# Optimization experiments

Measured on AMD Instinct MI355X. Metric: run time of the kernel, lower is better.

## Reference

```python
import jax, jax.numpy as jnp
import numpy as np

NUM_EMBEDDINGS = 1024
EMBEDDING_DIM = 64
COMMITMENT_COST = 0.25


def setup_inputs() -> dict:
    key = jax.random.key(0)
    k1, k2 = jax.random.split(key)
    inputs = jax.random.normal(k1, (64, 32, 32, EMBEDDING_DIM), dtype=jnp.float32)
    # torch init is uniform(-1/K, 1/K); scale accordingly
    weight = jax.random.uniform(
        k2, (NUM_EMBEDDINGS, EMBEDDING_DIM), dtype=jnp.float32,
        minval=-1.0 / NUM_EMBEDDINGS, maxval=1.0 / NUM_EMBEDDINGS)
    return {"inputs": inputs, "weight": weight}


def reference(inputs, weight):
    input_shape = inputs.shape
    flat = inputs.reshape(-1, EMBEDDING_DIM)               # [N, D]
    distances = (jnp.sum(flat ** 2, axis=1, keepdims=True)
                 + jnp.sum(weight ** 2, axis=1)
                 - 2.0 * flat @ weight.T)                   # [N, K]
    encoding_indices = jnp.argmin(distances, axis=1)        # [N]
    # gather codes (equivalent to one-hot @ weight, but as a direct gather)
    quantized = weight[encoding_indices].reshape(input_shape)

    e_latent_loss = jnp.mean((jax.lax.stop_gradient(quantized) - inputs) ** 2)
    q_latent_loss = jnp.mean((quantized - jax.lax.stop_gradient(inputs)) ** 2)
    loss = q_latent_loss + COMMITMENT_COST * e_latent_loss

    # straight-through estimator
    quantized_ste = inputs + jax.lax.stop_gradient(quantized - inputs)

    # perplexity (equivalent to mean over the one-hot encodings)
    n_tokens = flat.shape[0]
    counts = jax.ops.segment_sum(
        jnp.ones((n_tokens,), jnp.float32), encoding_indices,
        num_segments=NUM_EMBEDDINGS)
    avg_probs = counts / n_tokens
    perplexity = jnp.exp(-jnp.sum(avg_probs * jnp.log(avg_probs + 1e-10)))

    indices_for_transformer = encoding_indices.reshape(input_shape[0], -1)
    return (loss, quantized_ste, perplexity, indices_for_transformer)
```

## Files before the change

kernel.cpp:

```cpp
#include <hip/hip_runtime.h>
#include <cstdint>
#include <cstddef>

#define N_TOKENS 65536
#define DIM 64
#define K_CODES 1024
#define NTH 256

#define OFF_Q 1
#define OFF_PERP 4194305
#define OFF_IDX 4194306

#define MARGIN 1.5e-4f

#define WS_LOSS   0
#define WS_FCNT   8
#define WS_COUNTS 16
#define WS_WHI    4112
#define WS_WLO    135184
#define WS_S2     266256
#define WS_FLIST  270352

typedef __attribute__((ext_vector_type(8))) short  s16x8;
typedef __attribute__((ext_vector_type(4))) float  f32x4;

__device__ __forceinline__ float fmulr(float a, float b){ return __fmul_rn(a,b); }
__device__ __forceinline__ float faddr(float a, float b){ return __fadd_rn(a,b); }

__device__ __forceinline__ unsigned short f2bf(float f) {
    unsigned u = __float_as_uint(f);
    unsigned r = u + 0x7fffu + ((u >> 16) & 1u);
    return (unsigned short)(r >> 16);
}
__device__ __forceinline__ float bf2f(unsigned short h) {
    return __uint_as_float(((unsigned)h) << 16);
}
__device__ __forceinline__ unsigned keyf(float f) {
    unsigned u = __float_as_uint(f);
    return u ^ ((u & 0x80000000u) ? 0xffffffffu : 0x80000000u);
}

__device__ float sumsq64_np(const float* __restrict__ p) {
    float s[16];
    #pragma unroll
    for (int l = 0; l < 16; ++l) {
        float a0 = fmulr(p[l],      p[l]);
        float a1 = fmulr(p[l + 16], p[l + 16]);
        float a2 = fmulr(p[l + 32], p[l + 32]);
        float a3 = fmulr(p[l + 48], p[l + 48]);
        s[l] = faddr(faddr(a0, a1), faddr(a2, a3));
    }
    #pragma unroll
    for (int len = 8; len >= 1; len >>= 1)
        #pragma unroll
        for (int l = 0; l < len; ++l)
            s[l] = faddr(s[l], s[l + len]);
    return s[0];
}

__device__ __forceinline__ void async_copy16(const void* g, void* l) {
    __builtin_amdgcn_global_load_lds(
        (const __attribute__((address_space(1))) void*)g,
        (__attribute__((address_space(3))) void*)l, 16, 0, 0);
}

__global__ void vq_prep(const float* __restrict__ W, unsigned short* __restrict__ Whi,
                        unsigned short* __restrict__ Wlo, float* __restrict__ s2g,
                        int* __restrict__ counts, int* __restrict__ gfcount,
                        double* __restrict__ loss_acc) {
    int gid = blockIdx.x * NTH + threadIdx.x;
    for (int e = gid; e < K_CODES * DIM; e += 16384) {
        float x = W[e];
        unsigned short hi = f2bf(x);
        unsigned short lo = f2bf(__fsub_rn(x, bf2f(hi)));
        int j = e >> 6, k = e & 63;
        int pos = j * 64 + (((k >> 3) ^ (j & 7)) << 3) + (k & 7);
        Whi[pos] = hi; Wlo[pos] = lo;
    }
    if (gid < K_CODES) { s2g[gid] = sumsq64_np(W + gid * 64); counts[gid] = 0; }
    if (gid == 0) { *loss_acc = 0.0; *gfcount = 0; }
}

__global__ __launch_bounds__(NTH, 3)
void vq_main(const float* __restrict__ X, const float* __restrict__ W,
             const unsigned short* __restrict__ WhiG, const unsigned short* __restrict__ WloG,
             const float* __restrict__ s2g, float* __restrict__ out,
             double* __restrict__ loss_acc, int* __restrict__ counts,
             int* __restrict__ gfcount, unsigned short* __restrict__ gflist) {
    __shared__ __align__(16) unsigned short xs_hi[64 * 64];
    __shared__ __align__(16) unsigned short xs_lo[64 * 64];
    __shared__ __align__(16) unsigned short ws_hi[128 * 64];
    __shared__ __align__(16) unsigned short ws_lo[128 * 64];
    __shared__ int fidx[64];
    __shared__ int flist[64];
    __shared__ int fcount, gbaseS;
    __shared__ double lred[4];

    const int tid  = threadIdx.x;
    const int lane = tid & 63, wave = tid >> 6;
    const int quad = lane >> 4, lrow = lane & 15;
    const int t0   = blockIdx.x * 64;

    if (tid == 0) fcount = 0;

    #pragma unroll
    for (int i = 0; i < 2; ++i) {
        int g = tid + NTH * i;
        int t = g >> 3, kb = g & 7;
        const float* src = X + (size_t)(t0 + t) * DIM + kb * 8;
        float v[8];
        *(f32x4*)v       = *(const f32x4*)src;
        *(f32x4*)(v + 4) = *(const f32x4*)(src + 4);
        unsigned short h[8], l[8];
        #pragma unroll
        for (int k = 0; k < 8; ++k) {
            h[k] = f2bf(v[k]);
            l[k] = f2bf(__fsub_rn(v[k], bf2f(h[k])));
        }
        int base = t * 64 + ((kb ^ (t & 7)) << 3);
        *(s16x8*)&xs_hi[base] = *(s16x8*)h;
        *(s16x8*)&xs_lo[base] = *(s16x8*)l;
    }
    __syncthreads();

    const int tf = wave * 16 + lrow;
    const int sA = tf & 7;
    s16x8 a_h0 = *(const s16x8*)&xs_hi[tf * 64 + (((0 + quad) ^ sA) << 3)];
    s16x8 a_h1 = *(const s16x8*)&xs_hi[tf * 64 + (((4 + quad) ^ sA) << 3)];
    s16x8 a_l0 = *(const s16x8*)&xs_lo[tf * 64 + (((0 + quad) ^ sA) << 3)];
    s16x8 a_l1 = *(const s16x8*)&xs_lo[tf * 64 + (((4 + quad) ^ sA) << 3)];

    float r1v[4], r2v[4]; int r1i[4];
    #pragma unroll
    for (int r = 0; r < 4; ++r) { r1v[r] = 3.4e38f; r2v[r] = 3.4e38f; r1i[r] = 0x7fffffff; }

    for (int ch = 0; ch < 8; ++ch) {
        __syncthreads();
        {
            const char* ghb = (const char*)WhiG + ch * 16384;
            const char* glb = (const char*)WloG + ch * 16384;
            char* lhb = (char*)ws_hi + wave * 1024;
            char* llb = (char*)ws_lo + wave * 1024;
            #pragma unroll
            for (int i = 0; i < 4; ++i) {
                int off = i * 4096 + tid * 16;
                async_copy16(ghb + off, lhb + i * 4096);
                async_copy16(glb + off, llb + i * 4096);
            }
        }
        __syncthreads();

        #pragma unroll
        for (int g = 0; g < 2; ++g) {
            #pragma unroll
            for (int t4 = 0; t4 < 4; ++t4) {
                int jl = g * 64 + t4 * 16 + lrow;
                int sB = jl & 7;
                s16x8 b_h0 = *(const s16x8*)&ws_hi[jl * 64 + (((0 + quad) ^ sB) << 3)];
                s16x8 b_h1 = *(const s16x8*)&ws_hi[jl * 64 + (((4 + quad) ^ sB) << 3)];
                s16x8 b_l0 = *(const s16x8*)&ws_lo[jl * 64 + (((0 + quad) ^ sB) << 3)];
                s16x8 b_l1 = *(const s16x8*)&ws_lo[jl * 64 + (((4 + quad) ^ sB) << 3)];
                f32x4 acc = {0.f, 0.f, 0.f, 0.f};
                acc = __builtin_amdgcn_mfma_f32_16x16x32_bf16(a_h0, b_h0, acc, 0, 0, 0);
                acc = __builtin_amdgcn_mfma_f32_16x16x32_bf16(a_h1, b_h1, acc, 0, 0, 0);
                acc = __builtin_amdgcn_mfma_f32_16x16x32_bf16(a_h0, b_l0, acc, 0, 0, 0);
                acc = __builtin_amdgcn_mfma_f32_16x16x32_bf16(a_h1, b_l1, acc, 0, 0, 0);
                acc = __builtin_amdgcn_mfma_f32_16x16x32_bf16(a_l0, b_h0, acc, 0, 0, 0);
                acc = __builtin_amdgcn_mfma_f32_16x16x32_bf16(a_l1, b_h1, acc, 0, 0, 0);
                int jcode = ch * 128 + jl;
                float s2v = s2g[jcode];
                #pragma unroll
                for (int r = 0; r < 4; ++r) {
                    float d = __builtin_fmaf(-2.0f, acc[r], s2v);
                    bool lt = d < r1v[r];
                    float old1 = r1v[r];
                    float sec  = lt ? old1 : d;
                    r2v[r] = fminf(r2v[r], sec);
                    r1v[r] = lt ? d : r1v[r];
                    r1i[r] = lt ? jcode : r1i[r];
                }
            }
        }
    }

    #pragma unroll
    for (int m = 1; m <= 8; m <<= 1) {
        #pragma unroll
        for (int r = 0; r < 4; ++r) {
            float o1v = __shfl_xor(r1v[r], m, 64);
            int   o1i = __shfl_xor(r1i[r], m, 64);
            float o2v = __shfl_xor(r2v[r], m, 64);
            bool take = (o1v < r1v[r]) || (o1v == r1v[r] && o1i < r1i[r]);
            float loser = take ? r1v[r] : o1v;
            r2v[r] = fminf(fminf(r2v[r], o2v), loser);
            if (take) { r1v[r] = o1v; r1i[r] = o1i; }
        }
    }
    if (lrow == 0) {
        #pragma unroll
        for (int r = 0; r < 4; ++r) {
            int t = wave * 16 + quad * 4 + r;
            bool fb = (r2v[r] - r1v[r]) < MARGIN;
            fidx[t] = fb ? (r1i[r] | (int)0x80000000) : r1i[r];
            if (fb) { int p = atomicAdd(&fcount, 1); flist[p] = t; }
        }
    }
    __syncthreads();

    double lsum = 0.0;
    #pragma unroll
    for (int i = 0; i < 16; ++i) {
        int e = tid + NTH * i;
        int t = e >> 6, dd = e & 63;
        int iv = fidx[t];
        if (iv >= 0) {
            float q = W[iv * 64 + dd];
            float x = X[(size_t)(t0 + t) * 64 + dd];
            out[(size_t)OFF_Q + (size_t)(t0 + t) * 64 + dd] = q;
            float df = __fsub_rn(q, x);
            lsum += (double)fmulr(df, df);
        }
    }
    #pragma unroll
    for (int off = 32; off >= 1; off >>= 1) lsum += __shfl_down(lsum, off, 64);
    if (lane == 0) lred[wave] = lsum;
    if (tid < 64) {
        int iv = fidx[tid];
        if (iv >= 0) {
            atomicAdd(&counts[iv], 1);
            out[(size_t)OFF_IDX + t0 + tid] = (float)iv;
        }
    }
    if (tid == 0) gbaseS = atomicAdd(gfcount, fcount);
    __syncthreads();
    if (tid < fcount) gflist[gbaseS + tid] = (unsigned short)(t0 + flist[tid]);
    if (tid == 0) atomicAdd(loss_acc, lred[0] + lred[1] + lred[2] + lred[3]);
}

#define FGT 16
#define FBC 256

__global__ __launch_bounds__(NTH, 2)
void vq_fallback(const float* __restrict__ X, const float* __restrict__ W,
                 const float* __restrict__ s2g, const int* __restrict__ gfcount,
                 const unsigned short* __restrict__ gflist, float* __restrict__ out,
                 double* __restrict__ loss_acc, int* __restrict__ counts) {
    int count = *gfcount;
    int base = blockIdx.x * FGT;
    if (base >= count) return;
    int nt = min(FGT, count - base);

    __shared__ __align__(16) float xsf[FGT * 64];
    __shared__ __align__(16) float wsf[FBC * 64];
    __shared__ float s1f[FGT];
    __shared__ unsigned long long redf[FGT * 32];
    __shared__ int gidx[FGT];
    __shared__ double lredf[4];

    const int tid = threadIdx.x;
    const int lane = tid & 63, wave = tid >> 6;
    const int r = tid & 7, c = tid >> 3;

    if (tid < nt * 16) {
        int t = tid >> 4, kb4 = tid & 15;
        int tok = gflist[base + t];
        f32x4 v = *(const f32x4*)(X + (size_t)tok * 64 + kb4 * 4);
        *(f32x4*)&xsf[t * 64 + ((kb4 ^ (t & 7)) << 2)] = v;
    }
    if (tid < nt) s1f[tid] = sumsq64_np(X + (size_t)gflist[base + tid] * 64);

    unsigned long long best0 = ~0ULL, best1 = ~0ULL;
    const int ta = 2 * r, tb = 2 * r + 1;

    for (int ch = 0; ch < K_CODES / FBC; ++ch) {
        __syncthreads();
        #pragma unroll
        for (int i = 0; i < 16; ++i) {
            int e = tid + NTH * i;
            int jl = e >> 4, kb4 = e & 15;
            f32x4 v = *(const f32x4*)(W + (size_t)(ch * FBC + jl) * 64 + kb4 * 4);
            *(f32x4*)&wsf[jl * 64 + ((kb4 ^ ((jl >> 3) & 7)) << 2)] = v;
        }
        __syncthreads();

        float acc[2][8];
        #pragma unroll
        for (int m = 0; m < 8; ++m) { acc[0][m] = 0.f; acc[1][m] = 0.f; }

        #pragma unroll
        for (int kb4 = 0; kb4 < 16; ++kb4) {
            f32x4 xa = *(const f32x4*)&xsf[ta * 64 + ((kb4 ^ (ta & 7)) << 2)];
            f32x4 xb = *(const f32x4*)&xsf[tb * 64 + ((kb4 ^ (tb & 7)) << 2)];
            #pragma unroll
            for (int m = 0; m < 8; ++m) {
                int jl = 8 * c + m;
                f32x4 wv = *(const f32x4*)&wsf[jl * 64 + ((kb4 ^ (c & 7)) << 2)];
                acc[0][m] = __builtin_fmaf(xa[0], wv[0], acc[0][m]);
                acc[0][m] = __builtin_fmaf(xa[1], wv[1], acc[0][m]);
                acc[0][m] = __builtin_fmaf(xa[2], wv[2], acc[0][m]);
                acc[0][m] = __builtin_fmaf(xa[3], wv[3], acc[0][m]);
                acc[1][m] = __builtin_fmaf(xb[0], wv[0], acc[1][m]);
                acc[1][m] = __builtin_fmaf(xb[1], wv[1], acc[1][m]);
                acc[1][m] = __builtin_fmaf(xb[2], wv[2], acc[1][m]);
                acc[1][m] = __builtin_fmaf(xb[3], wv[3], acc[1][m]);
            }
        }
        #pragma unroll
        for (int m = 0; m < 8; ++m) {
            int jcode = ch * FBC + 8 * c + m;
            float s2v = s2g[jcode];
            float d0 = faddr(faddr(s1f[ta], s2v), fmulr(-2.0f, acc[0][m]));
            float d1 = faddr(faddr(s1f[tb], s2v), fmulr(-2.0f, acc[1][m]));
            unsigned long long p0 = ((unsigned long long)keyf(d0) << 32) | (unsigned)jcode;
            unsigned long long p1 = ((unsigned long long)keyf(d1) << 32) | (unsigned)jcode;
            best0 = p0 < best0 ? p0 : best0;
            best1 = p1 < best1 ? p1 : best1;
        }
    }
    redf[ta * 32 + c] = best0;
    redf[tb * 32 + c] = best1;
    __syncthreads();
    if (tid < FGT) {
        unsigned long long b = redf[tid * 32];
        #pragma unroll
        for (int cc = 1; cc < 32; ++cc) {
            unsigned long long v = redf[tid * 32 + cc];
            b = v < b ? v : b;
        }
        int idx = (int)(b & 0xffffffffu);
        gidx[tid] = idx;
        if (tid < nt) {
            int tok = gflist[base + tid];
            out[(size_t)OFF_IDX + tok] = (float)idx;
            atomicAdd(&counts[idx], 1);
        }
    }
    __syncthreads();
    double lsum = 0.0;
    #pragma unroll
    for (int i = 0; i < 4; ++i) {
        int e = tid + NTH * i;
        int t = e >> 6, dd = e & 63;
        if (t < nt) {
            int tok = gflist[base + t];
            int idx = gidx[t];
            float q = W[idx * 64 + dd];
            float x = X[(size_t)tok * 64 + dd];
            out[(size_t)OFF_Q + (size_t)tok * 64 + dd] = q;
            float df = __fsub_rn(q, x);
            lsum += (double)fmulr(df, df);
        }
    }
    #pragma unroll
    for (int off = 32; off >= 1; off >>= 1) lsum += __shfl_down(lsum, off, 64);
    if (lane == 0) lredf[wave] = lsum;
    __syncthreads();
    if (tid == 0) atomicAdd(loss_acc, lredf[0] + lredf[1] + lredf[2] + lredf[3]);
}

__global__ void vq_final(const int* __restrict__ counts,
                         const double* __restrict__ loss_acc,
                         float* __restrict__ out) {
    __shared__ double hred[4];
    int tid = threadIdx.x;
    double h = 0.0;
    for (int j = tid; j < K_CODES; j += 256) {
        double p = (double)counts[j] / 65536.0;
        h += p * log(p + 1e-10);
    }
    #pragma unroll
    for (int off = 32; off >= 1; off >>= 1) h += __shfl_down(h, off, 64);
    if ((tid & 63) == 0) hred[tid >> 6] = h;
    __syncthreads();
    if (tid == 0) {
        double H = hred[0] + hred[1] + hred[2] + hred[3];
        out[OFF_PERP] = (float)exp(-H);
        double ls = *loss_acc;
        float Lf = (float)(ls / 4194304.0);
        out[0] = faddr(Lf, fmulr(0.25f, Lf));
    }
}

extern "C" void kernel_launch(void* const* d_in, const int* in_sizes, int n_in,
                              void* d_out, int out_size, void* d_ws, size_t ws_size,
                              hipStream_t stream) {
    const float* X = (const float*)d_in[0];
    const float* W = (const float*)d_in[1];
    float* out = (float*)d_out;
    char* ws = (char*)d_ws;
    double* loss_acc = (double*)(ws + WS_LOSS);
    int* gfcount = (int*)(ws + WS_FCNT);
    int* counts = (int*)(ws + WS_COUNTS);
    unsigned short* Whi = (unsigned short*)(ws + WS_WHI);
    unsigned short* Wlo = (unsigned short*)(ws + WS_WLO);
    float* s2g = (float*)(ws + WS_S2);
    unsigned short* gflist = (unsigned short*)(ws + WS_FLIST);

    vq_prep<<<64, NTH, 0, stream>>>(W, Whi, Wlo, s2g, counts, gfcount, loss_acc);
    vq_main<<<N_TOKENS / 64, NTH, 0, stream>>>(X, W, Whi, Wlo, s2g, out,
                                               loss_acc, counts, gfcount, gflist);
    vq_fallback<<<N_TOKENS / FGT, NTH, 0, stream>>>(X, W, s2g, gfcount, gflist,
                                                    out, loss_acc, counts);
    vq_final<<<1, NTH, 0, stream>>>(counts, loss_acc, out);
}
```

Before: 177.3 us.

## Double-buffer codebook chunks, 128 tokens per block, retile fallback kernel

The main kernel now handles 128 tokens per block, with two 16-row A fragments per wave, so each codebook tile loaded into LDS is reused twice. Codebook chunks are 64 codes and double-buffered with async copies, so the next chunk loads while the current one computes, and each chunk iteration needs one barrier instead of two. The -0.5*||e||^2 term is folded into the MFMA accumulator init, and the per-code norms are staged once in LDS. The fallback kernel is retiled to 64 tokens x 128 codes with 4x8 register blocking, and the epilogue loads and stores are vectorised to float4. The cost is more registers and LDS per block (occupancy hint lowered from 3 to 2) and half as many main-kernel blocks.

```diff
diff --git a/kernel.cpp b/kernel.cpp
--- a/kernel.cpp
+++ b/kernel.cpp
@@ -6,6 +6,8 @@
 #define DIM 64
 #define K_CODES 1024
 #define NTH 256
+#define TPB 128
+#define NCH 16
 
 #define OFF_Q 1
 #define OFF_PERP 4194305
@@ -34,10 +36,6 @@
 }
 __device__ __forceinline__ float bf2f(unsigned short h) {
     return __uint_as_float(((unsigned)h) << 16);
-}
-__device__ __forceinline__ unsigned keyf(float f) {
-    unsigned u = __float_as_uint(f);
-    return u ^ ((u & 0x80000000u) ? 0xffffffffu : 0x80000000u);
 }
 
 __device__ float sumsq64_np(const float* __restrict__ p) {
@@ -81,30 +79,43 @@
     if (gid == 0) { *loss_acc = 0.0; *gfcount = 0; }
 }
 
-__global__ __launch_bounds__(NTH, 3)
+__global__ __launch_bounds__(NTH, 2)
 void vq_main(const float* __restrict__ X, const float* __restrict__ W,
              const unsigned short* __restrict__ WhiG, const unsigned short* __restrict__ WloG,
              const float* __restrict__ s2g, float* __restrict__ out,
              double* __restrict__ loss_acc, int* __restrict__ counts,
              int* __restrict__ gfcount, unsigned short* __restrict__ gflist) {
-    __shared__ __align__(16) unsigned short xs_hi[64 * 64];
-    __shared__ __align__(16) unsigned short xs_lo[64 * 64];
-    __shared__ __align__(16) unsigned short ws_hi[128 * 64];
-    __shared__ __align__(16) unsigned short ws_lo[128 * 64];
-    __shared__ int fidx[64];
-    __shared__ int flist[64];
+    __shared__ __align__(16) unsigned short xs_hi[TPB * 64];
+    __shared__ __align__(16) unsigned short xs_lo[TPB * 64];
+    __shared__ __align__(16) unsigned short ws_hi[2][64 * 64];
+    __shared__ __align__(16) unsigned short ws_lo[2][64 * 64];
+    __shared__ __align__(16) float s2s[K_CODES];
+    __shared__ int fidx[TPB];
+    __shared__ int flist[TPB];
     __shared__ int fcount, gbaseS;
     __shared__ double lred[4];
 
     const int tid  = threadIdx.x;
     const int lane = tid & 63, wave = tid >> 6;
     const int quad = lane >> 4, lrow = lane & 15;
-    const int t0   = blockIdx.x * 64;
+    const int t0   = blockIdx.x * TPB;
 
     if (tid == 0) fcount = 0;
 
-    #pragma unroll
-    for (int i = 0; i < 2; ++i) {
+    {
+        const char* gh = (const char*)WhiG;
+        const char* gl = (const char*)WloG;
+        char* lh = (char*)&ws_hi[0][0] + wave * 1024;
+        char* ll = (char*)&ws_lo[0][0] + wave * 1024;
+        #pragma unroll
+        for (int i = 0; i < 2; ++i) {
+            async_copy16(gh + i * 4096 + tid * 16, lh + i * 4096);
+            async_copy16(gl + i * 4096 + tid * 16, ll + i * 4096);
+        }
+    }
+    *(f32x4*)&s2s[tid * 4] = *(const f32x4*)&s2g[tid * 4];
+    #pragma unroll
+    for (int i = 0; i < 4; ++i) {
         int g = tid + NTH * i;
         int t = g >> 3, kb = g & 7;
         const float* src = X + (size_t)(t0 + t) * DIM + kb * 8;
@@ -123,85 +134,91 @@
     }
     __syncthreads();
 
-    const int tf = wave * 16 + lrow;
-    const int sA = tf & 7;
-    s16x8 a_h0 = *(const s16x8*)&xs_hi[tf * 64 + (((0 + quad) ^ sA) << 3)];
-    s16x8 a_h1 = *(const s16x8*)&xs_hi[tf * 64 + (((4 + quad) ^ sA) << 3)];
-    s16x8 a_l0 = *(const s16x8*)&xs_lo[tf * 64 + (((0 + quad) ^ sA) << 3)];
-    s16x8 a_l1 = *(const s16x8*)&xs_lo[tf * 64 + (((4 + quad) ^ sA) << 3)];
-
-    float r1v[4], r2v[4]; int r1i[4];
-    #pragma unroll
-    for (int r = 0; r < 4; ++r) { r1v[r] = 3.4e38f; r2v[r] = 3.4e38f; r1i[r] = 0x7fffffff; }
-
-    for (int ch = 0; ch < 8; ++ch) {
-        __syncthreads();
-        {
-            const char* ghb = (const char*)WhiG + ch * 16384;
-            const char* glb = (const char*)WloG + ch * 16384;
-            char* lhb = (char*)ws_hi + wave * 1024;
-            char* llb = (char*)ws_lo + wave * 1024;
-            #pragma unroll
-            for (int i = 0; i < 4; ++i) {
-                int off = i * 4096 + tid * 16;
-                async_copy16(ghb + off, lhb + i * 4096);
-                async_copy16(glb + off, llb + i * 4096);
+    s16x8 a_h0[2], a_h1[2], a_l0[2], a_l1[2];
+    #pragma unroll
+    for (int rt = 0; rt < 2; ++rt) {
+        int tf = wave * 32 + rt * 16 + lrow;
+        int sA = tf & 7;
+        a_h0[rt] = *(const s16x8*)&xs_hi[tf * 64 + (((0 + quad) ^ sA) << 3)];
+        a_h1[rt] = *(const s16x8*)&xs_hi[tf * 64 + (((4 + quad) ^ sA) << 3)];
+        a_l0[rt] = *(const s16x8*)&xs_lo[tf * 64 + (((0 + quad) ^ sA) << 3)];
+        a_l1[rt] = *(const s16x8*)&xs_lo[tf * 64 + (((4 + quad) ^ sA) << 3)];
+    }
+
+    float r1v[8], r2v[8]; int r1i[8];
+    #pragma unroll
+    for (int ri = 0; ri < 8; ++ri) { r1v[ri] = 3.4e38f; r2v[ri] = 3.4e38f; r1i[ri] = 0x7fffffff; }
+
+    for (int ch = 0; ch < NCH; ++ch) {
+        const int buf = ch & 1;
+        if (ch < NCH - 1) {
+            const char* gh = (const char*)WhiG + (ch + 1) * 8192;
+            const char* gl = (const char*)WloG + (ch + 1) * 8192;
+            char* lh = (char*)&ws_hi[buf ^ 1][0] + wave * 1024;
+            char* ll = (char*)&ws_lo[buf ^ 1][0] + wave * 1024;
+            #pragma unroll
+            for (int i = 0; i < 2; ++i) {
+                async_copy16(gh + i * 4096 + tid * 16, lh + i * 4096);
+                async_copy16(gl + i * 4096 + tid * 16, ll + i * 4096);
             }
         }
-        __syncthreads();
-
-        #pragma unroll
-        for (int g = 0; g < 2; ++g) {
-            #pragma unroll
-            for (int t4 = 0; t4 < 4; ++t4) {
-                int jl = g * 64 + t4 * 16 + lrow;
-                int sB = jl & 7;
-                s16x8 b_h0 = *(const s16x8*)&ws_hi[jl * 64 + (((0 + quad) ^ sB) << 3)];
-                s16x8 b_h1 = *(const s16x8*)&ws_hi[jl * 64 + (((4 + quad) ^ sB) << 3)];
-                s16x8 b_l0 = *(const s16x8*)&ws_lo[jl * 64 + (((0 + quad) ^ sB) << 3)];
-                s16x8 b_l1 = *(const s16x8*)&ws_lo[jl * 64 + (((4 + quad) ^ sB) << 3)];
-                f32x4 acc = {0.f, 0.f, 0.f, 0.f};
-                acc = __builtin_amdgcn_mfma_f32_16x16x32_bf16(a_h0, b_h0, acc, 0, 0, 0);
-                acc = __builtin_amdgcn_mfma_f32_16x16x32_bf16(a_h1, b_h1, acc, 0, 0, 0);
-                acc = __builtin_amdgcn_mfma_f32_16x16x32_bf16(a_h0, b_l0, acc, 0, 0, 0);
-                acc = __builtin_amdgcn_mfma_f32_16x16x32_bf16(a_h1, b_l1, acc, 0, 0, 0);
-                acc = __builtin_amdgcn_mfma_f32_16x16x32_bf16(a_l0, b_h0, acc, 0, 0, 0);
-                acc = __builtin_amdgcn_mfma_f32_16x16x32_bf16(a_l1, b_h1, acc, 0, 0, 0);
-                int jcode = ch * 128 + jl;
-                float s2v = s2g[jcode];
+        #pragma unroll
+        for (int ct = 0; ct < 4; ++ct) {
+            int lc = ct * 16 + lrow;
+            int sB = lrow & 7;
+            const unsigned short* bh = &ws_hi[buf][lc * 64];
+            const unsigned short* bl = &ws_lo[buf][lc * 64];
+            s16x8 b_h0 = *(const s16x8*)&bh[((0 + quad) ^ sB) << 3];
+            s16x8 b_h1 = *(const s16x8*)&bh[((4 + quad) ^ sB) << 3];
+            s16x8 b_l0 = *(const s16x8*)&bl[((0 + quad) ^ sB) << 3];
+            s16x8 b_l1 = *(const s16x8*)&bl[((4 + quad) ^ sB) << 3];
+            int jcode = ch * 64 + lc;
+            float s2v = s2s[jcode];
+            float ainit = fmulr(-0.5f, s2v);
+            #pragma unroll
+            for (int rt = 0; rt < 2; ++rt) {
+                f32x4 acc = {ainit, ainit, ainit, ainit};
+                acc = __builtin_amdgcn_mfma_f32_16x16x32_bf16(a_h0[rt], b_h0, acc, 0, 0, 0);
+                acc = __builtin_amdgcn_mfma_f32_16x16x32_bf16(a_h1[rt], b_h1, acc, 0, 0, 0);
+                acc = __builtin_amdgcn_mfma_f32_16x16x32_bf16(a_h0[rt], b_l0, acc, 0, 0, 0);
+                acc = __builtin_amdgcn_mfma_f32_16x16x32_bf16(a_h1[rt], b_l1, acc, 0, 0, 0);
+                acc = __builtin_amdgcn_mfma_f32_16x16x32_bf16(a_l0[rt], b_h0, acc, 0, 0, 0);
+                acc = __builtin_amdgcn_mfma_f32_16x16x32_bf16(a_l1[rt], b_h1, acc, 0, 0, 0);
                 #pragma unroll
                 for (int r = 0; r < 4; ++r) {
-                    float d = __builtin_fmaf(-2.0f, acc[r], s2v);
-                    bool lt = d < r1v[r];
-                    float old1 = r1v[r];
-                    float sec  = lt ? old1 : d;
-                    r2v[r] = fminf(r2v[r], sec);
-                    r1v[r] = lt ? d : r1v[r];
-                    r1i[r] = lt ? jcode : r1i[r];
+                    float d = fmulr(-2.0f, acc[r]);
+                    int ri = rt * 4 + r;
+                    bool lt = d < r1v[ri];
+                    float sec = lt ? r1v[ri] : d;
+                    r2v[ri] = fminf(r2v[ri], sec);
+                    r1v[ri] = lt ? d : r1v[ri];
+                    r1i[ri] = lt ? jcode : r1i[ri];
                 }
             }
         }
+        __syncthreads();
     }
 
     #pragma unroll
     for (int m = 1; m <= 8; m <<= 1) {
         #pragma unroll
-        for (int r = 0; r < 4; ++r) {
-            float o1v = __shfl_xor(r1v[r], m, 64);
-            int   o1i = __shfl_xor(r1i[r], m, 64);
-            float o2v = __shfl_xor(r2v[r], m, 64);
-            bool take = (o1v < r1v[r]) || (o1v == r1v[r] && o1i < r1i[r]);
-            float loser = take ? r1v[r] : o1v;
-            r2v[r] = fminf(fminf(r2v[r], o2v), loser);
-            if (take) { r1v[r] = o1v; r1i[r] = o1i; }
+        for (int ri = 0; ri < 8; ++ri) {
+            float o1v = __shfl_xor(r1v[ri], m, 64);
+            int   o1i = __shfl_xor(r1i[ri], m, 64);
+            float o2v = __shfl_xor(r2v[ri], m, 64);
+            bool take = (o1v < r1v[ri]) || (o1v == r1v[ri] && o1i < r1i[ri]);
+            float loser = take ? r1v[ri] : o1v;
+            r2v[ri] = fminf(fminf(r2v[ri], o2v), loser);
+            if (take) { r1v[ri] = o1v; r1i[ri] = o1i; }
         }
     }
     if (lrow == 0) {
         #pragma unroll
-        for (int r = 0; r < 4; ++r) {
-            int t = wave * 16 + quad * 4 + r;
-            bool fb = (r2v[r] - r1v[r]) < MARGIN;
-            fidx[t] = fb ? (r1i[r] | (int)0x80000000) : r1i[r];
+        for (int ri = 0; ri < 8; ++ri) {
+            int rt = ri >> 2, r = ri & 3;
+            int t = wave * 32 + rt * 16 + quad * 4 + r;
+            bool fb = (r2v[ri] - r1v[ri]) < MARGIN;
+            fidx[t] = fb ? (r1i[ri] | (int)0x80000000) : r1i[ri];
             if (fb) { int p = atomicAdd(&fcount, 1); flist[p] = t; }
         }
     }
@@ -209,22 +226,25 @@
 
     double lsum = 0.0;
     #pragma unroll
-    for (int i = 0; i < 16; ++i) {
-        int e = tid + NTH * i;
-        int t = e >> 6, dd = e & 63;
+    for (int i = 0; i < 8; ++i) {
+        int e4 = tid + NTH * i;
+        int t = e4 >> 4, d4 = (e4 & 15) * 4;
         int iv = fidx[t];
         if (iv >= 0) {
-            float q = W[iv * 64 + dd];
-            float x = X[(size_t)(t0 + t) * 64 + dd];
-            out[(size_t)OFF_Q + (size_t)(t0 + t) * 64 + dd] = q;
-            float df = __fsub_rn(q, x);
-            lsum += (double)fmulr(df, df);
+            f32x4 q = *(const f32x4*)&W[iv * 64 + d4];
+            f32x4 x = *(const f32x4*)&X[(size_t)(t0 + t) * 64 + d4];
+            *(f32x4*)&out[(size_t)OFF_Q + (size_t)(t0 + t) * 64 + d4] = q;
+            #pragma unroll
+            for (int c = 0; c < 4; ++c) {
+                float df = __fsub_rn(q[c], x[c]);
+                lsum += (double)fmulr(df, df);
+            }
         }
     }
     #pragma unroll
     for (int off = 32; off >= 1; off >>= 1) lsum += __shfl_down(lsum, off, 64);
     if (lane == 0) lred[wave] = lsum;
-    if (tid < 64) {
+    if (tid < TPB) {
         int iv = fidx[tid];
         if (iv >= 0) {
             atomicAdd(&counts[iv], 1);
@@ -237,97 +257,106 @@
     if (tid == 0) atomicAdd(loss_acc, lred[0] + lred[1] + lred[2] + lred[3]);
 }
 
-#define FGT 16
-#define FBC 256
-
-__global__ __launch_bounds__(NTH, 2)
+__global__ __launch_bounds__(NTH, 3)
 void vq_fallback(const float* __restrict__ X, const float* __restrict__ W,
                  const float* __restrict__ s2g, const int* __restrict__ gfcount,
                  const unsigned short* __restrict__ gflist, float* __restrict__ out,
                  double* __restrict__ loss_acc, int* __restrict__ counts) {
     int count = *gfcount;
-    int base = blockIdx.x * FGT;
+    int base = blockIdx.x * 64;
     if (base >= count) return;
-    int nt = min(FGT, count - base);
-
-    __shared__ __align__(16) float xsf[FGT * 64];
-    __shared__ __align__(16) float wsf[FBC * 64];
-    __shared__ float s1f[FGT];
-    __shared__ unsigned long long redf[FGT * 32];
-    __shared__ int gidx[FGT];
+    int nt = min(64, count - base);
+
+    __shared__ __align__(16) float xsf[64 * 64];
+    __shared__ __align__(16) float wsf[128 * 64];
+    __shared__ float s1f[64];
+    __shared__ int gidx[64];
     __shared__ double lredf[4];
 
     const int tid = threadIdx.x;
     const int lane = tid & 63, wave = tid >> 6;
-    const int r = tid & 7, c = tid >> 3;
-
-    if (tid < nt * 16) {
-        int t = tid >> 4, kb4 = tid & 15;
-        int tok = gflist[base + t];
-        f32x4 v = *(const f32x4*)(X + (size_t)tok * 64 + kb4 * 4);
-        *(f32x4*)&xsf[t * 64 + ((kb4 ^ (t & 7)) << 2)] = v;
+    const int r = tid & 15, c = tid >> 4;
+
+    #pragma unroll
+    for (int i = 0; i < 4; ++i) {
+        int idx = tid + NTH * i;
+        int t = idx >> 4, kb = idx & 15;
+        int tok = gflist[base + (t < nt ? t : 0)];
+        f32x4 v = *(const f32x4*)(X + (size_t)tok * 64 + kb * 4);
+        *(f32x4*)&xsf[t * 64 + ((kb ^ ((t >> 2) & 7)) << 2)] = v;
     }
     if (tid < nt) s1f[tid] = sumsq64_np(X + (size_t)gflist[base + tid] * 64);
 
-    unsigned long long best0 = ~0ULL, best1 = ~0ULL;
-    const int ta = 2 * r, tb = 2 * r + 1;
-
-    for (int ch = 0; ch < K_CODES / FBC; ++ch) {
+    float runVal[4]; int runIdx[4];
+    #pragma unroll
+    for (int i = 0; i < 4; ++i) { runVal[i] = 3.4e38f; runIdx[i] = 0; }
+
+    for (int ch = 0; ch < 8; ++ch) {
         __syncthreads();
         #pragma unroll
-        for (int i = 0; i < 16; ++i) {
-            int e = tid + NTH * i;
-            int jl = e >> 4, kb4 = e & 15;
-            f32x4 v = *(const f32x4*)(W + (size_t)(ch * FBC + jl) * 64 + kb4 * 4);
-            *(f32x4*)&wsf[jl * 64 + ((kb4 ^ ((jl >> 3) & 7)) << 2)] = v;
+        for (int i = 0; i < 8; ++i) {
+            int idx = tid + NTH * i;
+            int jl = idx >> 4, kb = idx & 15;
+            f32x4 v = *(const f32x4*)(W + (size_t)(ch * 128 + jl) * 64 + kb * 4);
+            *(f32x4*)&wsf[jl * 64 + ((kb ^ ((jl >> 3) & 7)) << 2)] = v;
         }
         __syncthreads();
 
-        float acc[2][8];
-        #pragma unroll
-        for (int m = 0; m < 8; ++m) { acc[0][m] = 0.f; acc[1][m] = 0.f; }
-
-        #pragma unroll
-        for (int kb4 = 0; kb4 < 16; ++kb4) {
-            f32x4 xa = *(const f32x4*)&xsf[ta * 64 + ((kb4 ^ (ta & 7)) << 2)];
-            f32x4 xb = *(const f32x4*)&xsf[tb * 64 + ((kb4 ^ (tb & 7)) << 2)];
+        float acc[4][8];
+        #pragma unroll
+        for (int i = 0; i < 4; ++i)
+            #pragma unroll
+            for (int m = 0; m < 8; ++m) acc[i][m] = 0.0f;
+
+        #pragma unroll
+        for (int kb = 0; kb < 16; ++kb) {
+            f32x4 xv[4], wv[8];
+            #pragma unroll
+            for (int i = 0; i < 4; ++i)
+                xv[i] = *(const f32x4*)&xsf[(4 * r + i) * 64 + ((kb ^ (r & 7)) << 2)];
+            #pragma unroll
+            for (int m = 0; m < 8; ++m)
+                wv[m] = *(const f32x4*)&wsf[(8 * c + m) * 64 + ((kb ^ (c & 7)) << 2)];
+            #pragma unroll
+            for (int i = 0; i < 4; ++i)
+                #pragma unroll
+                for (int m = 0; m < 8; ++m) {
+                    acc[i][m] = __builtin_fmaf(xv[i][0], wv[m][0], acc[i][m]);
+                    acc[i][m] = __builtin_fmaf(xv[i][1], wv[m][1], acc[i][m]);
+                    acc[i][m] = __builtin_fmaf(xv[i][2], wv[m][2], acc[i][m]);
+                    acc[i][m] = __builtin_fmaf(xv[i][3], wv[m][3], acc[i][m]);
+                }
+        }
+        #pragma unroll
+        for (int i = 0; i < 4; ++i) {
+            float s1v = s1f[4 * r + i];
             #pragma unroll
             for (int m = 0; m < 8; ++m) {
                 int jl = 8 * c + m;
-                f32x4 wv = *(const f32x4*)&wsf[jl * 64 + ((kb4 ^ (c & 7)) << 2)];
-                acc[0][m] = __builtin_fmaf(xa[0], wv[0], acc[0][m]);
-                acc[0][m] = __builtin_fmaf(xa[1], wv[1], acc[0][m]);
-                acc[0][m] = __builtin_fmaf(xa[2], wv[2], acc[0][m]);
-                acc[0][m] = __builtin_fmaf(xa[3], wv[3], acc[0][m]);
-                acc[1][m] = __builtin_fmaf(xb[0], wv[0], acc[1][m]);
-                acc[1][m] = __builtin_fmaf(xb[1], wv[1], acc[1][m]);
-                acc[1][m] = __builtin_fmaf(xb[2], wv[2], acc[1][m]);
-                acc[1][m] = __builtin_fmaf(xb[3], wv[3], acc[1][m]);
+                float d = faddr(faddr(s1v, s2g[ch * 128 + jl]), fmulr(-2.0f, acc[i][m]));
+                if (d < runVal[i]) { runVal[i] = d; runIdx[i] = ch * 128 + jl; }
             }
         }
-        #pragma unroll
-        for (int m = 0; m < 8; ++m) {
-            int jcode = ch * FBC + 8 * c + m;
-            float s2v = s2g[jcode];
-            float d0 = faddr(faddr(s1f[ta], s2v), fmulr(-2.0f, acc[0][m]));
-            float d1 = faddr(faddr(s1f[tb], s2v), fmulr(-2.0f, acc[1][m]));
-            unsigned long long p0 = ((unsigned long long)keyf(d0) << 32) | (unsigned)jcode;
-            unsigned long long p1 = ((unsigned long long)keyf(d1) << 32) | (unsigned)jcode;
-            best0 = p0 < best0 ? p0 : best0;
-            best1 = p1 < best1 ? p1 : best1;
-        }
-    }
-    redf[ta * 32 + c] = best0;
-    redf[tb * 32 + c] = best1;
-    __syncthreads();
-    if (tid < FGT) {
-        unsigned long long b = redf[tid * 32];
-        #pragma unroll
-        for (int cc = 1; cc < 32; ++cc) {
-            unsigned long long v = redf[tid * 32 + cc];
-            b = v < b ? v : b;
-        }
-        int idx = (int)(b & 0xffffffffu);
+    }
+
+    __syncthreads();
+    unsigned long long* red = (unsigned long long*)wsf;
+    #pragma unroll
+    for (int i = 0; i < 4; ++i) {
+        unsigned long long pk =
+            ((unsigned long long)__float_as_uint(runVal[i]) << 32) |
+            (unsigned long long)(unsigned int)runIdx[i];
+        red[(4 * r + i) * 16 + c] = pk;
+    }
+    __syncthreads();
+    if (tid < 64) {
+        unsigned long long best = red[tid * 16];
+        #pragma unroll
+        for (int cc = 1; cc < 16; ++cc) {
+            unsigned long long v = red[tid * 16 + cc];
+            best = (v < best) ? v : best;
+        }
+        int idx = (int)(best & 0xffffffffu);
         gidx[tid] = idx;
         if (tid < nt) {
             int tok = gflist[base + tid];
@@ -339,16 +368,19 @@
     double lsum = 0.0;
     #pragma unroll
     for (int i = 0; i < 4; ++i) {
-        int e = tid + NTH * i;
-        int t = e >> 6, dd = e & 63;
+        int e4 = tid + NTH * i;
+        int t = e4 >> 4, d4 = (e4 & 15) * 4;
         if (t < nt) {
             int tok = gflist[base + t];
             int idx = gidx[t];
-            float q = W[idx * 64 + dd];
-            float x = X[(size_t)tok * 64 + dd];
-            out[(size_t)OFF_Q + (size_t)tok * 64 + dd] = q;
-            float df = __fsub_rn(q, x);
-            lsum += (double)fmulr(df, df);
+            f32x4 q = *(const f32x4*)&W[idx * 64 + d4];
+            f32x4 x = *(const f32x4*)&X[(size_t)tok * 64 + d4];
+            *(f32x4*)&out[(size_t)OFF_Q + (size_t)tok * 64 + d4] = q;
+            #pragma unroll
+            for (int cc = 0; cc < 4; ++cc) {
+                float df = __fsub_rn(q[cc], x[cc]);
+                lsum += (double)fmulr(df, df);
+            }
         }
     }
     #pragma unroll
@@ -397,9 +429,9 @@
     unsigned short* gflist = (unsigned short*)(ws + WS_FLIST);
 
     vq_prep<<<64, NTH, 0, stream>>>(W, Whi, Wlo, s2g, counts, gfcount, loss_acc);
-    vq_main<<<N_TOKENS / 64, NTH, 0, stream>>>(X, W, Whi, Wlo, s2g, out,
-                                               loss_acc, counts, gfcount, gflist);
-    vq_fallback<<<N_TOKENS / FGT, NTH, 0, stream>>>(X, W, s2g, gfcount, gflist,
-                                                    out, loss_acc, counts);
+    vq_main<<<N_TOKENS / TPB, NTH, 0, stream>>>(X, W, Whi, Wlo, s2g, out,
+                                                loss_acc, counts, gfcount, gflist);
+    vq_fallback<<<N_TOKENS / 64, NTH, 0, stream>>>(X, W, s2g, gfcount, gflist,
+                                                   out, loss_acc, counts);
     vq_final<<<1, NTH, 0, stream>>>(counts, loss_acc, out);
 }
```

Measured after the change: 171.4 us. 3.4% less time.
